# Optimization experiments

Hardware: AMD Instinct MI355X
Metric: run time of the kernel (lower is better)

The kernel has to match this reference:

```python
import jax, jax.numpy as jnp
import numpy as np

DIM = 384
EPS = 1e-12  # F.normalize default eps


def setup_inputs() -> dict:
    key = jax.random.key(0)
    ks = jax.random.split(key, 6)
    b, c, h, w = 4, DIM, 64, 64
    x = jax.random.normal(ks[0], (b, c, h, w), dtype=jnp.float32)
    gamma = jnp.ones((c,), dtype=jnp.float32)  # WanRMS_norm gamma, init ones
    # 1x1 convs are per-pixel linear maps: [out_c, in_c] weight + bias
    w_qkv = jax.random.normal(ks[1], (3 * c, c), dtype=jnp.float32) * (1.0 / np.sqrt(c))
    b_qkv = jax.random.normal(ks[2], (3 * c,), dtype=jnp.float32) * 0.01
    w_proj = jax.random.normal(ks[3], (c, c), dtype=jnp.float32) * (1.0 / np.sqrt(c))
    b_proj = jax.random.normal(ks[4], (c,), dtype=jnp.float32) * 0.01
    return {"x": x, "gamma": gamma, "w_qkv": w_qkv, "b_qkv": b_qkv,
            "w_proj": w_proj, "b_proj": b_proj}


def reference(x, gamma, w_qkv, b_qkv, w_proj, b_proj):
    b, c, h, w = x.shape
    identity = x
    # WanRMS_norm: F.normalize over channel dim * sqrt(dim) * gamma
    l2 = jnp.sqrt(jnp.sum(x * x, axis=1, keepdims=True))
    xn = x / jnp.maximum(l2, EPS) * jnp.sqrt(jnp.float32(c)) * gamma[None, :, None, None]
    # 1x1 conv qkv: [b, 3c, h, w]
    qkv = jnp.einsum("bchw,oc->bohw", xn, w_qkv) + b_qkv[None, :, None, None]
    # flatten spatial -> tokens: [b, 3c, s] -> q/k/v each [b, s, c]
    s = h * w
    qkv = qkv.reshape(b, 3 * c, s).transpose(0, 2, 1)  # [b, s, 3c]
    q, k, v = jnp.split(qkv, 3, axis=-1)
    # single-head scaled dot-product attention (non-causal, as in Wan SDPA call)
    scores = jnp.einsum("bqc,bkc->bqk", q, k) / jnp.sqrt(jnp.float32(c))
    attn = jax.nn.softmax(scores, axis=-1)
    out = jnp.einsum("bqk,bkc->bqc", attn, v)  # [b, s, c]
    out = out.transpose(0, 2, 1).reshape(b, c, h, w)
    # 1x1 proj conv + residual
    out = jnp.einsum("bchw,oc->bohw", out, w_proj) + b_proj[None, :, None, None]
    return out + identity
```

## Files before the change

kernel.cpp:

```cpp
#include <hip/hip_runtime.h>
#include <cstdint>
#include <cstddef>

typedef __bf16 bf16;
typedef __bf16 bf16x8 __attribute__((ext_vector_type(8)));
typedef float  f32x4 __attribute__((ext_vector_type(4)));
typedef float  f32x16 __attribute__((ext_vector_type(16)));
typedef int    i32x4 __attribute__((ext_vector_type(4)));
typedef int    i32x8 __attribute__((ext_vector_type(8)));

#define MFMA16(a, b, c) __builtin_amdgcn_mfma_f32_16x16x32_bf16((a), (b), (c), 0, 0, 0)
#define MFMA_MX(a, b, c) \
    __builtin_amdgcn_mfma_scale_f32_32x32x64_f8f6f4((a), (b), (c), 0, 0, 0, 0x7F, 0, 0x7F)

#if __has_builtin(__builtin_amdgcn_exp2f)
#define EXP2(x) __builtin_amdgcn_exp2f(x)
#else
#define EXP2(x) exp2f(x)
#endif

__device__ __forceinline__ uint8_t to_fp8(float v) {
    return (uint8_t)(__builtin_amdgcn_cvt_pk_fp8_f32(v, v, 0, false) & 0xff);
}

__device__ __forceinline__ i32x8 ld32(const void* p) {
    i32x4 a = *(const i32x4*)p;
    i32x4 b = *(const i32x4*)((const char*)p + 16);
    i32x8 r;
    r[0] = a[0]; r[1] = a[1]; r[2] = a[2]; r[3] = a[3];
    r[4] = b[0]; r[5] = b[1]; r[6] = b[2]; r[7] = b[3];
    return r;
}

__device__ __forceinline__ void gload16(const void* g, void* l) {
    __builtin_amdgcn_global_load_lds(
        (const __attribute__((address_space(1))) unsigned int*)g,
        (__attribute__((address_space(3))) unsigned int*)l,
        16, 0, 0);
}

__global__ __launch_bounds__(256) void norm_kernel(
    const float* __restrict__ x, const float* __restrict__ gamma,
    const float* __restrict__ wqkv, const float* __restrict__ wproj,
    bf16* __restrict__ xn, bf16* __restrict__ wq, bf16* __restrict__ wp)
{
    const int tid = threadIdx.x;
    const int blk = blockIdx.x;
    if (blk >= 256) {
        int t0 = (blk - 256) * 256 + tid;
        for (int t = t0; t < 1152 * 384 + 384 * 384; t += 128 * 256) {
            if (t < 1152 * 384) wq[t] = (bf16)wqkv[t];
            else                wp[t - 1152 * 384] = (bf16)wproj[t - 1152 * 384];
        }
        return;
    }
    __shared__ float sG[384];
    __shared__ float sS[4][64];
    __shared__ float sScale[64];
    const int w = tid >> 6, l = tid & 63;
    for (int i = tid; i < 384; i += 256) sG[i] = gamma[i];
    const int b = blk >> 6, p0 = (blk & 63) << 6;
    const float* xb = x + ((size_t)b * 384) * 4096 + p0 + l;
    const float* xc = xb + (size_t)(96 * w) * 4096;
    float s0 = 0.f, s1 = 0.f;
#pragma unroll 8
    for (int c = 0; c < 96; c += 2) {
        float v0 = xc[(size_t)c * 4096];
        float v1 = xc[(size_t)(c + 1) * 4096];
        s0 += v0 * v0; s1 += v1 * v1;
    }
    sS[w][l] = s0 + s1;
    __syncthreads();
    if (w == 0) {
        float t = (sS[0][l] + sS[1][l]) + (sS[2][l] + sS[3][l]);
        sScale[l] = 19.595917942265423f / fmaxf(sqrtf(t), 1e-12f);
    }
    __syncthreads();
    float sc = sScale[l];
    int tok = (b << 12) + p0 + l;
    bf16* o = xn + (size_t)tok * 384 + 96 * w;
    for (int c0 = 0; c0 < 96; c0 += 8) {
        bf16x8 v8;
#pragma unroll
        for (int j = 0; j < 8; ++j)
            v8[j] = (bf16)(xc[(size_t)(c0 + j) * 4096] * sc * sG[96 * w + c0 + j]);
        *(bf16x8*)(o + c0) = v8;
    }
}

__device__ __forceinline__ void gemm_core_bt(
    bf16* sA, bf16* sB,
    const bf16* __restrict__ A, const bf16* __restrict__ B,
    const float* __restrict__ bias_m, const float* __restrict__ bias_n,
    uint8_t* __restrict__ Cout, const int mode, const int ldc,
    const int m0, const int n0)
{
    const int tid = threadIdx.x;
    const int l = tid & 63, w = tid >> 6;
    const int lo = l & 15, hi = l >> 4;
    const int wm = w >> 1, wn = w & 1;

    f32x4 acc[4][4] = {};

    for (int kt = 0; kt < 6; ++kt) {
        __syncthreads();
        const int k0 = kt * 64;
#pragma unroll
        for (int i = 0; i < 5; ++i) {
            int ci = i * 256 + tid;
            if (ci < 1152) {
                int row = ci / 9, off = ci % 9;
                gload16(A + (size_t)(m0 + row) * 384 + k0 + off * 8, (char*)sA + ci * 16);
                gload16(B + (size_t)(n0 + row) * 384 + k0 + off * 8, (char*)sB + ci * 16);
            }
        }
        __syncthreads();
#pragma unroll
        for (int ks = 0; ks < 2; ++ks) {
            bf16x8 af[4], bfr[4];
#pragma unroll
            for (int t = 0; t < 4; ++t)
                af[t] = *(const bf16x8*)(sA + (wm * 64 + t * 16 + lo) * 72 + ks * 32 + hi * 8);
#pragma unroll
            for (int t = 0; t < 4; ++t)
                bfr[t] = *(const bf16x8*)(sB + (wn * 64 + t * 16 + lo) * 72 + ks * 32 + hi * 8);
#pragma unroll
            for (int rt = 0; rt < 4; ++rt)
#pragma unroll
                for (int ct = 0; ct < 4; ++ct)
                    acc[rt][ct] = MFMA16(af[rt], bfr[ct], acc[rt][ct]);
        }
    }

#pragma unroll
    for (int rt = 0; rt < 4; ++rt) {
#pragma unroll
        for (int ct = 0; ct < 4; ++ct) {
            int mb = m0 + wm * 64 + rt * 16 + hi * 4;
            int n  = n0 + wn * 64 + ct * 16 + lo;
            if (mode == 0) {
                float bn = bias_n[n];
#pragma unroll
                for (int r = 0; r < 4; ++r)
                    Cout[(size_t)(mb + r) * ldc + n] = to_fp8(acc[rt][ct][r] + bn);
            } else {
#pragma unroll
                for (int r = 0; r < 4; ++r)
                    Cout[(size_t)(mb + r) * ldc + n] = to_fp8(acc[rt][ct][r] + bias_m[mb + r]);
            }
        }
    }
}

__global__ __launch_bounds__(256) void gemm_qkv(
    const bf16* __restrict__ xn, const bf16* __restrict__ wq,
    const float* __restrict__ b_qkv, uint8_t* __restrict__ qkb,
    uint8_t* __restrict__ vtb)
{
    __shared__ bf16 sA[128 * 72];
    __shared__ bf16 sB[128 * 72];
    const int id = blockIdx.x;
    if (id < 768) {
        const int xcd = id & 7, s = id >> 3;
        gemm_core_bt(sA, sB, xn, wq, nullptr, b_qkv, qkb, 0, 768,
                     (xcd * 16 + s / 6) * 128, (s % 6) * 128);
    } else {
        const int t = id - 768;
        const int xcd = t & 7, s = t >> 3;
        gemm_core_bt(sA, sB, wq + (size_t)768 * 384, xn, b_qkv + 768, nullptr,
                     vtb, 1, 16384, (s % 3) * 128, (xcd * 16 + s / 3) * 128);
    }
}

__global__ __launch_bounds__(256) void gemm_proj(
    const bf16* __restrict__ wp, const bf16* __restrict__ p0,
    const bf16* __restrict__ p1, const float* __restrict__ ml,
    const float* __restrict__ b_proj, const float* __restrict__ x,
    float* __restrict__ out)
{
    __shared__ bf16 sA[128 * 72];
    __shared__ bf16 sB[128 * 72];
    const int tid = threadIdx.x;
    const int l = tid & 63, w = tid >> 6;
    const int lo = l & 15, hi = l >> 4;
    const int wm = w >> 1, wn = w & 1;
    const int id = blockIdx.x;
    const int xcd = id & 7, s = id >> 3;
    const int m0 = (s % 3) * 128, n0 = (xcd * 16 + s / 3) * 128;

    f32x4 acc[4][4] = {};

    for (int kt = 0; kt < 6; ++kt) {
        __syncthreads();
        const int k0 = kt * 64;
#pragma unroll
        for (int i = 0; i < 5; ++i) {
            int ci = i * 256 + tid;
            if (ci < 1152) {
                int row = ci / 9, off = ci % 9;
                gload16(wp + (size_t)(m0 + row) * 384 + k0 + off * 8, (char*)sA + ci * 16);
                int tok = n0 + row;
                float2 ml0 = *(const float2*)(ml + (size_t)tok * 2);
                float2 ml1 = *(const float2*)(ml + (size_t)(16384 + tok) * 2);
                float mM = fmaxf(ml0.x, ml1.x);
                float a0 = EXP2(ml0.x - mM), a1 = EXP2(ml1.x - mM);
                float inv = 1.0f / (a0 * ml0.y + a1 * ml1.y);
                float w0 = a0 * inv, w1 = a1 * inv;
                size_t boff = (size_t)tok * 384 + k0 + off * 8;
                bf16x8 v0 = *(const bf16x8*)(p0 + boff);
                bf16x8 v1 = *(const bf16x8*)(p1 + boff);
                bf16x8 r;
#pragma unroll
                for (int j = 0; j < 8; ++j)
                    r[j] = (bf16)((float)v0[j] * w0 + (float)v1[j] * w1);
                *(bf16x8*)((char*)sB + ci * 16) = r;
            }
        }
        __syncthreads();
#pragma unroll
        for (int ks = 0; ks < 2; ++ks) {
            bf16x8 af[4], bfr[4];
#pragma unroll
            for (int t = 0; t < 4; ++t)
                af[t] = *(const bf16x8*)(sA + (wm * 64 + t * 16 + lo) * 72 + ks * 32 + hi * 8);
#pragma unroll
            for (int t = 0; t < 4; ++t)
                bfr[t] = *(const bf16x8*)(sB + (wn * 64 + t * 16 + lo) * 72 + ks * 32 + hi * 8);
#pragma unroll
            for (int rt = 0; rt < 4; ++rt)
#pragma unroll
                for (int ct = 0; ct < 4; ++ct)
                    acc[rt][ct] = MFMA16(af[rt], bfr[ct], acc[rt][ct]);
        }
    }

#pragma unroll
    for (int rt = 0; rt < 4; ++rt) {
#pragma unroll
        for (int ct = 0; ct < 4; ++ct) {
            int mb = m0 + wm * 64 + rt * 16 + hi * 4;
            int n  = n0 + wn * 64 + ct * 16 + lo;
            int bb = n >> 12, p = n & 4095;
#pragma unroll
            for (int r = 0; r < 4; ++r) {
                int m = mb + r;
                size_t idx = ((size_t)(bb * 384 + m)) * 4096 + p;
                out[idx] = acc[rt][ct][r] + b_proj[m] + x[idx];
            }
        }
    }
}

__global__ __launch_bounds__(256, 2) void flash_kernel(
    const uint8_t* __restrict__ qk, const uint8_t* __restrict__ vt,
    bf16* __restrict__ op0, bf16* __restrict__ op1, float* __restrict__ ml)
{
    extern __shared__ char smem[];
    uint8_t* sbase = (uint8_t*)smem;
    const int tid = threadIdx.x;
    const int l = tid & 63, w = tid >> 6;
    const int l31 = l & 31, hi2 = l >> 5;
    const int wq = w >> 1, wd = w & 1;
    const int id = blockIdx.x;
    const int qt = id >> 3, bh = id & 7;
    const int b = bh >> 1, half = bh & 1;
    const int q0 = b * 4096 + qt * 64;
    const int kvbase = b * 4096 + half * 2048;
    const float SC = 0.07362217057594547f;
    const float THR = 108.664f;

    uint32_t ksrc[7];
#pragma unroll
    for (int i = 0; i < 7; ++i) {
        int ci = i * 256 + tid;
        int row = ci / 25, off = ci % 25;
        ksrc[i] = (uint32_t)((kvbase + row) * 768 + 384 + off * 16);
    }
#pragma unroll
    for (int i = 0; i < 7; ++i) {
        if (i < 6 || tid < 64) gload16(qk + ksrc[i], sbase + i * 4096 + tid * 16);
        ksrc[i] += 49152;
    }

    uint32_t voff[6];
#pragma unroll
    for (int dt = 0; dt < 6; ++dt)
        voff[dt] = (uint32_t)((wd * 192 + dt * 32 + l31) * 16384 + kvbase + hi2 * 32);

    i32x8 qf[6];
    {
        const uint8_t* qrow = qk + (size_t)(q0 + wq * 32 + l31) * 768 + hi2 * 32;
#pragma unroll
        for (int ksw = 0; ksw < 6; ++ksw)
            qf[ksw] = ld32(qrow + ksw * 64);
    }

    f32x16 o[6] = {};
    float m = -1e30f, lsum = 0.f;

    __syncthreads();

    int c = 0;
    for (int kt = 0; kt < 32; ++kt) {
        if (kt < 31) {
            uint8_t* dst = sbase + (c ^ 1) * 25600;
#pragma unroll
            for (int i = 0; i < 7; ++i) {
                if (i < 6 || tid < 64) gload16(qk + ksrc[i], dst + i * 4096 + tid * 16);
                ksrc[i] += 49152;
            }
        }
        i32x8 av[6];
#pragma unroll
        for (int dt = 0; dt < 6; ++dt) {
            av[dt] = ld32(vt + voff[dt]);
            voff[dt] += 64;
        }

        const uint8_t* sK = sbase + c * 25600;
        f32x16 s0 = {}, s1 = {};
        __builtin_amdgcn_s_setprio(1);
#pragma unroll
        for (int ksw = 0; ksw < 6; ++ksw) {
            i32x8 ak0 = ld32(sK + (size_t)l31 * 400 + ksw * 64 + hi2 * 32);
            i32x8 ak1 = ld32(sK + (size_t)(32 + l31) * 400 + ksw * 64 + hi2 * 32);
            s0 = MFMA_MX(ak0, qf[ksw], s0);
            s1 = MFMA_MX(ak1, qf[ksw], s1);
        }
        __builtin_amdgcn_s_setprio(0);

        float a0 = fmaxf(fmaxf(s0[0],  s0[1]),  fmaxf(s0[2],  s0[3]));
        float a1 = fmaxf(fmaxf(s0[4],  s0[5]),  fmaxf(s0[6],  s0[7]));
        float a2 = fmaxf(fmaxf(s0[8],  s0[9]),  fmaxf(s0[10], s0[11]));
        float a3 = fmaxf(fmaxf(s0[12], s0[13]), fmaxf(s0[14], s0[15]));
        float b0 = fmaxf(fmaxf(s1[0],  s1[1]),  fmaxf(s1[2],  s1[3]));
        float b1 = fmaxf(fmaxf(s1[4],  s1[5]),  fmaxf(s1[6],  s1[7]));
        float b2 = fmaxf(fmaxf(s1[8],  s1[9]),  fmaxf(s1[10], s1[11]));
        float b3 = fmaxf(fmaxf(s1[12], s1[13]), fmaxf(s1[14], s1[15]));
        float mx = fmaxf(fmaxf(fmaxf(a0, a1), fmaxf(a2, a3)),
                         fmaxf(fmaxf(b0, b1), fmaxf(b2, b3)));
        mx = fmaxf(mx, __shfl_xor(mx, 32));
        if (__any(mx > m + THR)) {
            float mn = fmaxf(m, mx);
            float alpha = EXP2((m - mn) * SC);
            m = mn;
            lsum *= alpha;
#pragma unroll
            for (int dt = 0; dt < 6; ++dt)
#pragma unroll
                for (int r = 0; r < 16; ++r) o[dt][r] *= alpha;
        }
        float p0[16], p1[16];
        float msc = m * SC;
        float rsa = 0.f, rsb = 0.f, rsc = 0.f, rsd = 0.f;
#pragma unroll
        for (int r = 0; r < 16; r += 4) {
            p0[r]     = EXP2(fmaf(s0[r],     SC, -msc)); rsa += p0[r];
            p0[r + 1] = EXP2(fmaf(s0[r + 1], SC, -msc)); rsb += p0[r + 1];
            p0[r + 2] = EXP2(fmaf(s0[r + 2], SC, -msc)); rsc += p0[r + 2];
            p0[r + 3] = EXP2(fmaf(s0[r + 3], SC, -msc)); rsd += p0[r + 3];
        }
#pragma unroll
        for (int r = 0; r < 16; r += 4) {
            p1[r]     = EXP2(fmaf(s1[r],     SC, -msc)); rsa += p1[r];
            p1[r + 1] = EXP2(fmaf(s1[r + 1], SC, -msc)); rsb += p1[r + 1];
            p1[r + 2] = EXP2(fmaf(s1[r + 2], SC, -msc)); rsc += p1[r + 2];
            p1[r + 3] = EXP2(fmaf(s1[r + 3], SC, -msc)); rsd += p1[r + 3];
        }
        float rs = (rsa + rsb) + (rsc + rsd);
        rs += __shfl_xor(rs, 32);
        lsum += rs;

        int pk0[4], pk1[4];
#pragma unroll
        for (int i = 0; i < 4; ++i) {
            int d = __builtin_amdgcn_cvt_pk_fp8_f32(p0[4 * i], p0[4 * i + 1], 0, false);
            pk0[i] = __builtin_amdgcn_cvt_pk_fp8_f32(p0[4 * i + 2], p0[4 * i + 3], d, true);
            d = __builtin_amdgcn_cvt_pk_fp8_f32(p1[4 * i], p1[4 * i + 1], 0, false);
            pk1[i] = __builtin_amdgcn_cvt_pk_fp8_f32(p1[4 * i + 2], p1[4 * i + 3], d, true);
        }
        i32x8 pf;
#pragma unroll
        for (int i = 0; i < 4; ++i) {
            int x0 = __shfl_xor(pk0[i], 32);
            int x1 = __shfl_xor(pk1[i], 32);
            int own = hi2 ? pk1[i] : pk0[i];
            int oth = hi2 ? x1 : x0;
            pf[2 * i]     = hi2 ? oth : own;
            pf[2 * i + 1] = hi2 ? own : oth;
        }

        __builtin_amdgcn_s_setprio(1);
#pragma unroll
        for (int dt = 0; dt < 6; ++dt)
            o[dt] = MFMA_MX(av[dt], pf, o[dt]);
        __builtin_amdgcn_s_setprio(0);

        __syncthreads();
        c ^= 1;
    }

    float* tr = (float*)(smem + w * 4608);
    bf16* dst = half ? op1 : op0;
#pragma unroll
    for (int dt = 0; dt < 6; ++dt) {
#pragma unroll
        for (int r = 0; r < 16; ++r) {
            int d32 = (r & 3) + 8 * (r >> 2) + 4 * hi2;
            tr[l31 * 36 + d32] = o[dt][r];
        }
        f32x4 v0 = *(f32x4*)(tr + l31 * 36 + hi2 * 16 + 0);
        f32x4 v1 = *(f32x4*)(tr + l31 * 36 + hi2 * 16 + 4);
        f32x4 v2 = *(f32x4*)(tr + l31 * 36 + hi2 * 16 + 8);
        f32x4 v3 = *(f32x4*)(tr + l31 * 36 + hi2 * 16 + 12);
        bf16x8 h0, h1;
#pragma unroll
        for (int j = 0; j < 4; ++j) {
            h0[j] = (bf16)v0[j]; h0[4 + j] = (bf16)v1[j];
            h1[j] = (bf16)v2[j]; h1[4 + j] = (bf16)v3[j];
        }
        size_t tok = (size_t)(q0 + wq * 32 + l31);
        bf16* drow = dst + tok * 384 + wd * 192 + dt * 32 + hi2 * 16;
        *(bf16x8*)(drow + 0) = h0;
        *(bf16x8*)(drow + 8) = h1;
    }
    if (wd == 0 && hi2 == 0) {
        int tok = q0 + wq * 32 + l31;
        ml[(size_t)(half * 16384 + tok) * 2 + 0] = m * SC;
        ml[(size_t)(half * 16384 + tok) * 2 + 1] = lsum;
    }
}

extern "C" void kernel_launch(void* const* d_in, const int* in_sizes, int n_in,
                              void* d_out, int out_size, void* d_ws, size_t ws_size,
                              hipStream_t stream) {
    const float* x      = (const float*)d_in[0];
    const float* gamma  = (const float*)d_in[1];
    const float* w_qkv  = (const float*)d_in[2];
    const float* b_qkv  = (const float*)d_in[3];
    const float* w_proj = (const float*)d_in[4];
    const float* b_proj = (const float*)d_in[5];
    float* out = (float*)d_out;

    char* ws = (char*)d_ws;
    bf16* xn  = (bf16*)ws;    ws += (size_t)16384 * 384 * 2;
    uint8_t* qkb = (uint8_t*)ws; ws += (size_t)16384 * 768;
    uint8_t* vtb = (uint8_t*)ws; ws += (size_t)384 * 16384;
    bf16* ob  = (bf16*)ws;    ws += (size_t)16384 * 384 * 2;
    bf16* wqb = (bf16*)ws;    ws += (size_t)1152 * 384 * 2;
    bf16* wpb = (bf16*)ws;    ws += (size_t)384 * 384 * 2;
    float* mlb = (float*)ws;  ws += (size_t)2 * 16384 * 2 * 4;

    (void)hipFuncSetAttribute((const void*)flash_kernel,
                              hipFuncAttributeMaxDynamicSharedMemorySize, 51200);

    norm_kernel<<<384, 256, 0, stream>>>(x, gamma, w_qkv, w_proj, xn, wqb, wpb);
    gemm_qkv<<<1152, 256, 0, stream>>>(xn, wqb, b_qkv, qkb, vtb);
    flash_kernel<<<512, 256, 51200, stream>>>(qkb, vtb, xn, ob, mlb);
    gemm_proj<<<384, 256, 0, stream>>>(wpb, xn, ob, mlb, b_proj, x, out);
}
```

Measured before the change: 289.9 us.

## Stage V tiles through LDS, reverse KV order, and coalesce norm output

The flash kernel now copies each V tile into shared memory with 16-byte async loads and reads MFMA operands from LDS, replacing per-lane 32-byte global loads. Half of the blocks walk their KV range in reverse, which looks aimed at spreading the memory-access pattern across blocks. The norm kernel keeps x values in registers and transposes through shared memory so the bf16 token-major output is written as coalesced 16-byte rows. This raises flash shared memory to 80KB, which may reduce occupancy below two blocks per CU, and adds an extra barrier per iteration because the V copy is not double-buffered.

```diff
diff --git a/kernel.cpp b/kernel.cpp
--- a/kernel.cpp
+++ b/kernel.cpp
@@ -57,17 +57,18 @@
     __shared__ float sG[384];
     __shared__ float sS[4][64];
     __shared__ float sScale[64];
+    __shared__ bf16  sT[64][392];
     const int w = tid >> 6, l = tid & 63;
     for (int i = tid; i < 384; i += 256) sG[i] = gamma[i];
     const int b = blk >> 6, p0 = (blk & 63) << 6;
-    const float* xb = x + ((size_t)b * 384) * 4096 + p0 + l;
-    const float* xc = xb + (size_t)(96 * w) * 4096;
+    const float* xc = x + ((size_t)(b * 384 + 96 * w)) * 4096 + p0 + l;
+    float v[96];
     float s0 = 0.f, s1 = 0.f;
-#pragma unroll 8
+#pragma unroll
     for (int c = 0; c < 96; c += 2) {
-        float v0 = xc[(size_t)c * 4096];
-        float v1 = xc[(size_t)(c + 1) * 4096];
-        s0 += v0 * v0; s1 += v1 * v1;
+        v[c]     = xc[(size_t)c * 4096];
+        v[c + 1] = xc[(size_t)(c + 1) * 4096];
+        s0 += v[c] * v[c]; s1 += v[c + 1] * v[c + 1];
     }
     sS[w][l] = s0 + s1;
     __syncthreads();
@@ -77,15 +78,21 @@
     }
     __syncthreads();
     float sc = sScale[l];
-    int tok = (b << 12) + p0 + l;
-    bf16* o = xn + (size_t)tok * 384 + 96 * w;
+#pragma unroll
     for (int c0 = 0; c0 < 96; c0 += 8) {
         bf16x8 v8;
 #pragma unroll
         for (int j = 0; j < 8; ++j)
-            v8[j] = (bf16)(xc[(size_t)(c0 + j) * 4096] * sc * sG[96 * w + c0 + j]);
-        *(bf16x8*)(o + c0) = v8;
-    }
+            v8[j] = (bf16)(v[c0 + j] * sc * sG[96 * w + c0 + j]);
+        *(bf16x8*)(&sT[l][96 * w + c0]) = v8;
+    }
+    __syncthreads();
+    const int r = tid >> 2, seg = tid & 3;
+    const bf16* srow = &sT[r][seg * 96];
+    bf16* drow = xn + (size_t)((b << 12) + p0 + r) * 384 + seg * 96;
+#pragma unroll
+    for (int j = 0; j < 12; ++j)
+        *(i32x4*)(drow + j * 8) = *(const i32x4*)(srow + j * 8);
 }
 
 __device__ __forceinline__ void gemm_core_bt(
@@ -257,6 +264,7 @@
 {
     extern __shared__ char smem[];
     uint8_t* sbase = (uint8_t*)smem;
+    uint8_t* sV = sbase + 51200;
     const int tid = threadIdx.x;
     const int l = tid & 63, w = tid >> 6;
     const int l31 = l & 31, hi2 = l >> 5;
@@ -264,8 +272,12 @@
     const int id = blockIdx.x;
     const int qt = id >> 3, bh = id & 7;
     const int b = bh >> 1, half = bh & 1;
-    const int q0 = b * 4096 + qt * 64;
+    const int q0 = b * 4096 + (qt & 63) * 64;
     const int kvbase = b * 4096 + half * 2048;
+    const int rev = (id >> 8) & 1;
+    const int kvstart = kvbase + (rev ? 31 * 64 : 0);
+    const int kstep = rev ? -49152 : 49152;
+    const int vstep = rev ? -64 : 64;
     const float SC = 0.07362217057594547f;
     const float THR = 108.664f;
 
@@ -274,18 +286,20 @@
     for (int i = 0; i < 7; ++i) {
         int ci = i * 256 + tid;
         int row = ci / 25, off = ci % 25;
-        ksrc[i] = (uint32_t)((kvbase + row) * 768 + 384 + off * 16);
+        ksrc[i] = (uint32_t)((kvstart + row) * 768 + 384 + off * 16);
+    }
+    uint32_t vsrc[8];
+#pragma unroll
+    for (int i = 0; i < 8; ++i) {
+        int ci = i * 256 + tid;
+        int row = ci / 5, off = ci % 5;
+        vsrc[i] = (uint32_t)(row * 16384 + kvstart + off * 16);
     }
 #pragma unroll
     for (int i = 0; i < 7; ++i) {
         if (i < 6 || tid < 64) gload16(qk + ksrc[i], sbase + i * 4096 + tid * 16);
-        ksrc[i] += 49152;
-    }
-
-    uint32_t voff[6];
-#pragma unroll
-    for (int dt = 0; dt < 6; ++dt)
-        voff[dt] = (uint32_t)((wd * 192 + dt * 32 + l31) * 16384 + kvbase + hi2 * 32);
+        ksrc[i] += (uint32_t)kstep;
+    }
 
     i32x8 qf[6];
     {
@@ -302,19 +316,18 @@
 
     int c = 0;
     for (int kt = 0; kt < 32; ++kt) {
+#pragma unroll
+        for (int i = 0; i < 8; ++i) {
+            if (i < 7 || tid < 128) gload16(vt + vsrc[i], sV + i * 4096 + tid * 16);
+            vsrc[i] += (uint32_t)vstep;
+        }
         if (kt < 31) {
             uint8_t* dst = sbase + (c ^ 1) * 25600;
 #pragma unroll
             for (int i = 0; i < 7; ++i) {
                 if (i < 6 || tid < 64) gload16(qk + ksrc[i], dst + i * 4096 + tid * 16);
-                ksrc[i] += 49152;
+                ksrc[i] += (uint32_t)kstep;
             }
-        }
-        i32x8 av[6];
-#pragma unroll
-        for (int dt = 0; dt < 6; ++dt) {
-            av[dt] = ld32(vt + voff[dt]);
-            voff[dt] += 64;
         }
 
         const uint8_t* sK = sbase + c * 25600;
@@ -390,10 +403,14 @@
             pf[2 * i + 1] = hi2 ? own : oth;
         }
 
+        __syncthreads();
+
         __builtin_amdgcn_s_setprio(1);
 #pragma unroll
-        for (int dt = 0; dt < 6; ++dt)
-            o[dt] = MFMA_MX(av[dt], pf, o[dt]);
+        for (int dt = 0; dt < 6; ++dt) {
+            i32x8 av = ld32(sV + (size_t)(wd * 192 + dt * 32 + l31) * 80 + hi2 * 32);
+            o[dt] = MFMA_MX(av, pf, o[dt]);
+        }
         __builtin_amdgcn_s_setprio(0);
 
         __syncthreads();
@@ -452,10 +469,10 @@
     float* mlb = (float*)ws;  ws += (size_t)2 * 16384 * 2 * 4;
 
     (void)hipFuncSetAttribute((const void*)flash_kernel,
-                              hipFuncAttributeMaxDynamicSharedMemorySize, 51200);
+                              hipFuncAttributeMaxDynamicSharedMemorySize, 81920);
 
     norm_kernel<<<384, 256, 0, stream>>>(x, gamma, w_qkv, w_proj, xn, wqb, wpb);
     gemm_qkv<<<1152, 256, 0, stream>>>(xn, wqb, b_qkv, qkb, vtb);
-    flash_kernel<<<512, 256, 51200, stream>>>(qkb, vtb, xn, ob, mlb);
+    flash_kernel<<<512, 256, 81920, stream>>>(qkb, vtb, xn, ob, mlb);
     gemm_proj<<<384, 256, 0, stream>>>(wpb, xn, ob, mlb, b_proj, x, out);
 }
```

New measurement: 236.6 us. 18.4% less time.
